# Kernel tuning notes

Hardware: AMD Instinct MI355X
Metric: run time of the kernel (lower is better)

The kernel has to match this reference:

```python
import jax, jax.numpy as jnp
import numpy as np

B, H, W, C = 1, 256, 256, 256  # pooled feature map, NHWC
OH, OW = 2 * H, 2 * W          # unpooled output spatial dims


def setup_inputs() -> dict:
    key = jax.random.key(0)
    val = jax.random.normal(key, (B, H, W, C), dtype=jnp.float32)
    # Canonical argmax indices: each pooled element maps to the top-left
    # corner of its 2x2 window in the flattened [OH, OW, C] output.
    h = jnp.arange(H, dtype=jnp.int32)[:, None, None]   # [H,1,1]
    w = jnp.arange(W, dtype=jnp.int32)[None, :, None]   # [1,W,1]
    c = jnp.arange(C, dtype=jnp.int32)[None, None, :]   # [1,1,C]
    index = ((2 * h) * OW + (2 * w)) * C + c            # [H,W,C]
    index = jnp.broadcast_to(index, (B, H, W, C))
    return {"val": val, "index": index}


def reference(val, index):
    # tf.scatter_nd into a flat buffer of size OH*OW*C (duplicates sum),
    # then reshape to [-1, OH, OW, C].
    flat = jnp.zeros((OH * OW * C,), dtype=val.dtype)
    flat = flat.at[index.reshape(-1)].add(val.reshape(-1))
    return flat.reshape(-1, OH, OW, C)
```

## Files before the change

### kernel.cpp

```cpp
#include <hip/hip_runtime.h>


typedef float  f32x4 __attribute__((ext_vector_type(4)));
typedef int    i32x4 __attribute__((ext_vector_type(4)));

__global__ void unpool_fused_kernel(const float* __restrict__ val,
                                    const int* __restrict__ idx,
                                    float* __restrict__ out, int n4) {
    const int tid = blockIdx.x * blockDim.x + threadIdx.x;
    if (tid >= n4) return;
    const f32x4 v  = __builtin_nontemporal_load(reinterpret_cast<const f32x4*>(val) + tid);
    const i32x4 id = __builtin_nontemporal_load(reinterpret_cast<const i32x4*>(idx) + tid);

    const int c4  = tid & 63;
    const int pix = tid >> 6;
    const int w   = pix & 255;
    const int h   = pix >> 8;

    const int p00 = h * 262144 + w * 512 + c4 * 4;
    const int p10 = p00 + 131072;

    f32x4* o = reinterpret_cast<f32x4*>(out);
    const f32x4 z = (f32x4)(0.f);

    if (id.x == p00 && id.y == p00 + 1 && id.z == p00 + 2 && id.w == p00 + 3) {
        __builtin_nontemporal_store(v, o + (p00 >> 2));
    } else {
        __builtin_nontemporal_store(z, o + (p00 >> 2));
        atomicAdd(out + id.x, v.x);
        atomicAdd(out + id.y, v.y);
        atomicAdd(out + id.z, v.z);
        atomicAdd(out + id.w, v.w);
    }
    __builtin_nontemporal_store(z, o + ((p00 + 256) >> 2));
    __builtin_nontemporal_store(z, o + (p10 >> 2));
    __builtin_nontemporal_store(z, o + ((p10 + 256) >> 2));
}

extern "C" void kernel_launch(void* const* d_in, const int* in_sizes, int n_in,
                              void* d_out, int out_size, void* d_ws, size_t ws_size,
                              hipStream_t stream) {
    const float* val = (const float*)d_in[0];
    const int*   idx = (const int*)d_in[1];
    float* out = (float*)d_out;

    const int n  = in_sizes[0];
    const int n4 = n / 4;
    const int block = 256;
    const int grid = (n4 + block - 1) / block;
    unpool_fused_kernel<<<grid, block, 0, stream>>>(val, idx, out, n4);
}
```

Measured before the change: 347.1 us.

## Switch unpool kernel to output-centric mapping with one thread per output vector

```diff
diff --git a/kernel.cpp b/kernel.cpp
--- a/kernel.cpp
+++ b/kernel.cpp
@@ -4,37 +4,41 @@
 typedef float  f32x4 __attribute__((ext_vector_type(4)));
 typedef int    i32x4 __attribute__((ext_vector_type(4)));
 
-__global__ void unpool_fused_kernel(const float* __restrict__ val,
-                                    const int* __restrict__ idx,
-                                    float* __restrict__ out, int n4) {
+__global__ __launch_bounds__(256) void unpool_outcentric_kernel(
+    const float* __restrict__ val,
+    const int*   __restrict__ idx,
+    float*       __restrict__ out,
+    int nq)
+{
     const int tid = blockIdx.x * blockDim.x + threadIdx.x;
-    if (tid >= n4) return;
-    const f32x4 v  = __builtin_nontemporal_load(reinterpret_cast<const f32x4*>(val) + tid);
-    const i32x4 id = __builtin_nontemporal_load(reinterpret_cast<const i32x4*>(idx) + tid);
-
-    const int c4  = tid & 63;
-    const int pix = tid >> 6;
-    const int w   = pix & 255;
-    const int h   = pix >> 8;
-
-    const int p00 = h * 262144 + w * 512 + c4 * 4;
-    const int p10 = p00 + 131072;
+    if (tid >= nq) return;
 
     f32x4* o = reinterpret_cast<f32x4*>(out);
     const f32x4 z = (f32x4)(0.f);
 
-    if (id.x == p00 && id.y == p00 + 1 && id.z == p00 + 2 && id.w == p00 + 3) {
-        __builtin_nontemporal_store(v, o + (p00 >> 2));
+    const int c4 = tid & 63;
+    const int ow = (tid >> 6) & 511;
+    const int oh = tid >> 15;
+
+    if ((oh | ow) & 1) {
+        __builtin_nontemporal_store(z, o + tid);
+        return;
+    }
+
+    const int qin = ((oh >> 1) << 14) + ((ow >> 1) << 6) + c4;
+    const f32x4 v  = __builtin_nontemporal_load(reinterpret_cast<const f32x4*>(val) + qin);
+    const i32x4 id = __builtin_nontemporal_load(reinterpret_cast<const i32x4*>(idx) + qin);
+
+    const int p = tid << 2;
+    if (__builtin_expect(id.x == p && id.y == p + 1 && id.z == p + 2 && id.w == p + 3, 1)) {
+        __builtin_nontemporal_store(v, o + tid);
     } else {
-        __builtin_nontemporal_store(z, o + (p00 >> 2));
+        __builtin_nontemporal_store(z, o + tid);
         atomicAdd(out + id.x, v.x);
         atomicAdd(out + id.y, v.y);
         atomicAdd(out + id.z, v.z);
         atomicAdd(out + id.w, v.w);
     }
-    __builtin_nontemporal_store(z, o + ((p00 + 256) >> 2));
-    __builtin_nontemporal_store(z, o + (p10 >> 2));
-    __builtin_nontemporal_store(z, o + ((p10 + 256) >> 2));
 }
 
 extern "C" void kernel_launch(void* const* d_in, const int* in_sizes, int n_in,
@@ -45,8 +49,8 @@
     float* out = (float*)d_out;
 
     const int n  = in_sizes[0];
-    const int n4 = n / 4;
+    const int nq = n;
     const int block = 256;
-    const int grid = (n4 + block - 1) / block;
-    unpool_fused_kernel<<<grid, block, 0, stream>>>(val, idx, out, n4);
+    const int grid  = (nq + block - 1) / block;
+    unpool_outcentric_kernel<<<grid, block, 0, stream>>>(val, idx, out, nq);
 }
```

New measurement: 336.3 us. -3.1%, faster.
